# Kernel optimization log

Measured on AMD Instinct MI355X. Metric: run time of the kernel, lower is better.

Reference implementation:

```python
import jax, jax.numpy as jnp
import numpy as np

V, E, C = 50000, 5000, 16
TAU = 0.5
EPS = 1e-08
SPARSITY = 0.02  # fraction of (v,e) incidences


def setup_inputs() -> dict:
    key = jax.random.key(0)
    k1, k2, k3, k4 = jax.random.split(key, 4)
    pred_s = jax.random.normal(k1, (V, C), dtype=jnp.float32)
    pred_t = jax.random.normal(k2, (V, C), dtype=jnp.float32)
    # binary incidence matrix; pin vertex 0 into every edge so deg_e > 0
    H = (jax.random.uniform(k3, (V, E)) < SPARSITY).astype(jnp.float32)
    H = H.at[0, :].set(1.0)
    e_mask = jax.random.randint(k4, (E,), 0, 2).astype(jnp.bool_)
    return {"pred_s": pred_s, "pred_t": pred_t, "H": H, "e_mask": e_mask}


def _v2e_mean(p, H, deg_e):
    # == einsum('vc,ve->ec', p, H @ diag(1/deg_e)) : column-normalized scatter-mean
    return jnp.einsum('ve,vc->ec', H, p) / deg_e[:, None]


def reference(pred_s, pred_t, H, e_mask):
    ps = jax.nn.softmax(pred_s, axis=1)   # [V, C]
    pt = jax.nn.softmax(pred_t, axis=1)   # [V, C]
    deg_e = H.sum(axis=0)                 # [E]
    log_s = jnp.log(_v2e_mean(ps, H, deg_e) / TAU + EPS)  # [E, C]
    log_t = jnp.log(_v2e_mean(pt, H, deg_e) / TAU + EPS)  # [E, C]
    # F.kl_div(input=log_s, target=log_t, log_target=True, reduction='batchmean')
    # restricted to masked edges; mask via weights to keep shapes static.
    kl = jnp.exp(log_t) * (log_t - log_s)                  # [E, C]
    m = e_mask.astype(kl.dtype)                            # [E]
    n_sel = jnp.maximum(m.sum(), 1.0)
    return (kl * m[:, None]).sum() / n_sel
```

## Files before the change

kernel.cpp:

```cpp
#include <hip/hip_runtime.h>

#define NV 50000
#define NE 5000
#define NC 16
#define TAU_INV 2.0f
#define EPS 1e-8f
#define VCHUNK 1000
#define NCHUNK 50

__global__ __launch_bounds__(256) void softmax_kernel(
    const float* __restrict__ pred_s, const float* __restrict__ pred_t,
    float* __restrict__ ps, float* __restrict__ pt) {
  int i = blockIdx.x * 256 + threadIdx.x;
  if (i >= 2 * NV) return;
  const float* src;
  float* dst;
  if (i < NV) { src = pred_s + (size_t)i * NC; dst = ps + (size_t)i * NC; }
  else        { int j = i - NV; src = pred_t + (size_t)j * NC; dst = pt + (size_t)j * NC; }
  float4 a = ((const float4*)src)[0];
  float4 b = ((const float4*)src)[1];
  float4 c = ((const float4*)src)[2];
  float4 d = ((const float4*)src)[3];
  float x[16] = {a.x,a.y,a.z,a.w, b.x,b.y,b.z,b.w, c.x,c.y,c.z,c.w, d.x,d.y,d.z,d.w};
  float mx = x[0];
#pragma unroll
  for (int k = 1; k < 16; ++k) mx = fmaxf(mx, x[k]);
  float sum = 0.f;
#pragma unroll
  for (int k = 0; k < 16; ++k) { x[k] = expf(x[k] - mx); sum += x[k]; }
  float inv = 1.f / sum;
#pragma unroll
  for (int k = 0; k < 16; ++k) x[k] *= inv;
  float4 o0 = {x[0], x[1], x[2], x[3]};
  float4 o1 = {x[4], x[5], x[6], x[7]};
  float4 o2 = {x[8], x[9], x[10], x[11]};
  float4 o3 = {x[12], x[13], x[14], x[15]};
  ((float4*)dst)[0] = o0;
  ((float4*)dst)[1] = o1;
  ((float4*)dst)[2] = o2;
  ((float4*)dst)[3] = o3;
}

__global__ __launch_bounds__(256) void accum_kernel(
    const float* __restrict__ H, const float* __restrict__ ps,
    const float* __restrict__ pt, float* __restrict__ acc) {
  int e = blockIdx.x * 256 + threadIdx.x;
  if (e >= NE) return;
  int v0 = blockIdx.y * VCHUNK;

  float deg = 0.f;
  float as[16], at[16];
#pragma unroll
  for (int k = 0; k < 16; ++k) { as[k] = 0.f; at[k] = 0.f; }

  const float* hp = H + (size_t)v0 * NE + e;
  for (int v = v0; v < v0 + VCHUNK; v += 4) {
    float h0 = hp[0];
    float h1 = hp[NE];
    float h2 = hp[2 * NE];
    float h3 = hp[3 * NE];
    hp += (size_t)4 * NE;
#pragma unroll
    for (int u = 0; u < 4; ++u) {
      float h = (u == 0) ? h0 : (u == 1) ? h1 : (u == 2) ? h2 : h3;
      const float* rs = ps + (size_t)(v + u) * NC;
      const float* rt = pt + (size_t)(v + u) * NC;
      float4 sA = ((const float4*)rs)[0];
      float4 sB = ((const float4*)rs)[1];
      float4 sC = ((const float4*)rs)[2];
      float4 sD = ((const float4*)rs)[3];
      float4 tA = ((const float4*)rt)[0];
      float4 tB = ((const float4*)rt)[1];
      float4 tC = ((const float4*)rt)[2];
      float4 tD = ((const float4*)rt)[3];
      float sv[16] = {sA.x,sA.y,sA.z,sA.w, sB.x,sB.y,sB.z,sB.w,
                      sC.x,sC.y,sC.z,sC.w, sD.x,sD.y,sD.z,sD.w};
      float tv[16] = {tA.x,tA.y,tA.z,tA.w, tB.x,tB.y,tB.z,tB.w,
                      tC.x,tC.y,tC.z,tC.w, tD.x,tD.y,tD.z,tD.w};
      deg += h;
#pragma unroll
      for (int k = 0; k < 16; ++k) as[k] = fmaf(h, sv[k], as[k]);
#pragma unroll
      for (int k = 0; k < 16; ++k) at[k] = fmaf(h, tv[k], at[k]);
    }
  }

  atomicAdd(&acc[e], deg);
#pragma unroll
  for (int k = 0; k < 16; ++k)
    atomicAdd(&acc[NE + (size_t)k * NE + e], as[k]);
#pragma unroll
  for (int k = 0; k < 16; ++k)
    atomicAdd(&acc[(size_t)17 * NE + (size_t)k * NE + e], at[k]);
}

__global__ __launch_bounds__(256) void kl_kernel(
    const float* __restrict__ acc, const unsigned char* __restrict__ e_mask,
    float* __restrict__ out) {
  __shared__ float snum[256];
  __shared__ float scnt[256];
  int t = threadIdx.x;
  float num = 0.f, cnt = 0.f;
  for (int e = t; e < NE; e += 256) {
    if (e_mask[e]) {
      float deg = acc[e];
      float invd = 1.f / deg;
      float kl = 0.f;
#pragma unroll
      for (int k = 0; k < 16; ++k) {
        float ms = acc[NE + (size_t)k * NE + e] * invd;
        float mt = acc[(size_t)17 * NE + (size_t)k * NE + e] * invd;
        float xs = ms * TAU_INV + EPS;
        float xt = mt * TAU_INV + EPS;
        kl += xt * (logf(xt) - logf(xs));
      }
      num += kl;
      cnt += 1.f;
    }
  }
  snum[t] = num;
  scnt[t] = cnt;
  __syncthreads();
  if (t == 0) {
    float n = 0.f, c2 = 0.f;
    for (int k = 0; k < 256; ++k) { n += snum[k]; c2 += scnt[k]; }
    out[0] = n / fmaxf(c2, 1.f);
  }
}

extern "C" void kernel_launch(void* const* d_in, const int* in_sizes, int n_in,
                              void* d_out, int out_size, void* d_ws, size_t ws_size,
                              hipStream_t stream) {
  const float* pred_s = (const float*)d_in[0];
  const float* pred_t = (const float*)d_in[1];
  const float* H      = (const float*)d_in[2];
  const unsigned char* e_mask = (const unsigned char*)d_in[3];

  float* ws = (float*)d_ws;
  float* ps  = ws;
  float* pt  = ws + (size_t)NV * NC;
  float* acc = ws + (size_t)2 * NV * NC;

  hipMemsetAsync(acc, 0, (size_t)33 * NE * sizeof(float), stream);
  softmax_kernel<<<dim3((2 * NV + 255) / 256), 256, 0, stream>>>(pred_s, pred_t, ps, pt);
  accum_kernel<<<dim3((NE + 255) / 256, NCHUNK), 256, 0, stream>>>(H, ps, pt, acc);
  kl_kernel<<<1, 256, 0, stream>>>(acc, e_mask, (float*)d_out);
}
```

Baseline: 1.451 ms.

## Interleave softmax outputs per vertex and simplify accumulation loop

The softmax outputs for the student and teacher predictions are now written into one interleaved buffer of 32 floats per vertex, so the accumulation kernel reads both rows from a single contiguous 128-byte region. The accumulation loop is restructured to step one vertex at a time with unroll 2, and gets a launch-bounds occupancy hint. Out-of-range threads are clamped rather than returning early, so every lane stays active through the loop and only the atomics are guarded. The final KL reduction now uses wavefront shuffles instead of a serial 256-element loop, which is minor next to the dominant read of the dense H matrix.

```diff
diff --git a/kernel.cpp b/kernel.cpp
--- a/kernel.cpp
+++ b/kernel.cpp
@@ -10,13 +10,13 @@
 
 __global__ __launch_bounds__(256) void softmax_kernel(
     const float* __restrict__ pred_s, const float* __restrict__ pred_t,
-    float* __restrict__ ps, float* __restrict__ pt) {
+    float* __restrict__ p) {
   int i = blockIdx.x * 256 + threadIdx.x;
   if (i >= 2 * NV) return;
   const float* src;
   float* dst;
-  if (i < NV) { src = pred_s + (size_t)i * NC; dst = ps + (size_t)i * NC; }
-  else        { int j = i - NV; src = pred_t + (size_t)j * NC; dst = pt + (size_t)j * NC; }
+  if (i < NV) { src = pred_s + (size_t)i * NC; dst = p + (size_t)i * 32; }
+  else        { int j = i - NV; src = pred_t + (size_t)j * NC; dst = p + (size_t)j * 32 + 16; }
   float4 a = ((const float4*)src)[0];
   float4 b = ((const float4*)src)[1];
   float4 c = ((const float4*)src)[2];
@@ -41,11 +41,11 @@
   ((float4*)dst)[3] = o3;
 }
 
-__global__ __launch_bounds__(256) void accum_kernel(
-    const float* __restrict__ H, const float* __restrict__ ps,
-    const float* __restrict__ pt, float* __restrict__ acc) {
-  int e = blockIdx.x * 256 + threadIdx.x;
-  if (e >= NE) return;
+__global__ __launch_bounds__(256, 4) void accum_kernel(
+    const float* __restrict__ H, const float* __restrict__ p,
+    float* __restrict__ acc) {
+  int te = blockIdx.x * 256 + threadIdx.x;
+  int e = te < NE ? te : NE - 1;
   int v0 = blockIdx.y * VCHUNK;
 
   float deg = 0.f;
@@ -53,52 +53,47 @@
 #pragma unroll
   for (int k = 0; k < 16; ++k) { as[k] = 0.f; at[k] = 0.f; }
 
-  const float* hp = H + (size_t)v0 * NE + e;
-  for (int v = v0; v < v0 + VCHUNK; v += 4) {
-    float h0 = hp[0];
-    float h1 = hp[NE];
-    float h2 = hp[2 * NE];
-    float h3 = hp[3 * NE];
-    hp += (size_t)4 * NE;
+  const float* __restrict__ hp = H + (size_t)v0 * NE + e;
+  const float* __restrict__ pp = p + (size_t)v0 * 32;
+
+#pragma unroll 2
+  for (int v = 0; v < VCHUNK; ++v) {
+    float h = hp[(size_t)v * NE];
+    float4 sA = ((const float4*)(pp + (size_t)v * 32))[0];
+    float4 sB = ((const float4*)(pp + (size_t)v * 32))[1];
+    float4 sC = ((const float4*)(pp + (size_t)v * 32))[2];
+    float4 sD = ((const float4*)(pp + (size_t)v * 32))[3];
+    float4 tA = ((const float4*)(pp + (size_t)v * 32))[4];
+    float4 tB = ((const float4*)(pp + (size_t)v * 32))[5];
+    float4 tC = ((const float4*)(pp + (size_t)v * 32))[6];
+    float4 tD = ((const float4*)(pp + (size_t)v * 32))[7];
+    float sv[16] = {sA.x,sA.y,sA.z,sA.w, sB.x,sB.y,sB.z,sB.w,
+                    sC.x,sC.y,sC.z,sC.w, sD.x,sD.y,sD.z,sD.w};
+    float tv[16] = {tA.x,tA.y,tA.z,tA.w, tB.x,tB.y,tB.z,tB.w,
+                    tC.x,tC.y,tC.z,tC.w, tD.x,tD.y,tD.z,tD.w};
+    deg += h;
 #pragma unroll
-    for (int u = 0; u < 4; ++u) {
-      float h = (u == 0) ? h0 : (u == 1) ? h1 : (u == 2) ? h2 : h3;
-      const float* rs = ps + (size_t)(v + u) * NC;
-      const float* rt = pt + (size_t)(v + u) * NC;
-      float4 sA = ((const float4*)rs)[0];
-      float4 sB = ((const float4*)rs)[1];
-      float4 sC = ((const float4*)rs)[2];
-      float4 sD = ((const float4*)rs)[3];
-      float4 tA = ((const float4*)rt)[0];
-      float4 tB = ((const float4*)rt)[1];
-      float4 tC = ((const float4*)rt)[2];
-      float4 tD = ((const float4*)rt)[3];
-      float sv[16] = {sA.x,sA.y,sA.z,sA.w, sB.x,sB.y,sB.z,sB.w,
-                      sC.x,sC.y,sC.z,sC.w, sD.x,sD.y,sD.z,sD.w};
-      float tv[16] = {tA.x,tA.y,tA.z,tA.w, tB.x,tB.y,tB.z,tB.w,
-                      tC.x,tC.y,tC.z,tC.w, tD.x,tD.y,tD.z,tD.w};
-      deg += h;
+    for (int k = 0; k < 16; ++k) as[k] = fmaf(h, sv[k], as[k]);
 #pragma unroll
-      for (int k = 0; k < 16; ++k) as[k] = fmaf(h, sv[k], as[k]);
-#pragma unroll
-      for (int k = 0; k < 16; ++k) at[k] = fmaf(h, tv[k], at[k]);
-    }
+    for (int k = 0; k < 16; ++k) at[k] = fmaf(h, tv[k], at[k]);
   }
 
-  atomicAdd(&acc[e], deg);
+  if (te < NE) {
+    atomicAdd(&acc[e], deg);
 #pragma unroll
-  for (int k = 0; k < 16; ++k)
-    atomicAdd(&acc[NE + (size_t)k * NE + e], as[k]);
+    for (int k = 0; k < 16; ++k)
+      atomicAdd(&acc[NE + (size_t)k * NE + e], as[k]);
 #pragma unroll
-  for (int k = 0; k < 16; ++k)
-    atomicAdd(&acc[(size_t)17 * NE + (size_t)k * NE + e], at[k]);
+    for (int k = 0; k < 16; ++k)
+      atomicAdd(&acc[(size_t)17 * NE + (size_t)k * NE + e], at[k]);
+  }
 }
 
 __global__ __launch_bounds__(256) void kl_kernel(
     const float* __restrict__ acc, const unsigned char* __restrict__ e_mask,
     float* __restrict__ out) {
-  __shared__ float snum[256];
-  __shared__ float scnt[256];
+  __shared__ float snum[4];
+  __shared__ float scnt[4];
   int t = threadIdx.x;
   float num = 0.f, cnt = 0.f;
   for (int e = t; e < NE; e += 256) {
@@ -118,12 +113,16 @@
       cnt += 1.f;
     }
   }
-  snum[t] = num;
-  scnt[t] = cnt;
+#pragma unroll
+  for (int off = 32; off > 0; off >>= 1) {
+    num += __shfl_down(num, off, 64);
+    cnt += __shfl_down(cnt, off, 64);
+  }
+  if ((t & 63) == 0) { snum[t >> 6] = num; scnt[t >> 6] = cnt; }
   __syncthreads();
   if (t == 0) {
-    float n = 0.f, c2 = 0.f;
-    for (int k = 0; k < 256; ++k) { n += snum[k]; c2 += scnt[k]; }
+    float n = snum[0] + snum[1] + snum[2] + snum[3];
+    float c2 = scnt[0] + scnt[1] + scnt[2] + scnt[3];
     out[0] = n / fmaxf(c2, 1.f);
   }
 }
@@ -137,12 +136,11 @@
   const unsigned char* e_mask = (const unsigned char*)d_in[3];
 
   float* ws = (float*)d_ws;
-  float* ps  = ws;
-  float* pt  = ws + (size_t)NV * NC;
-  float* acc = ws + (size_t)2 * NV * NC;
+  float* p   = ws;
+  float* acc = ws + (size_t)NV * 32;
 
   hipMemsetAsync(acc, 0, (size_t)33 * NE * sizeof(float), stream);
-  softmax_kernel<<<dim3((2 * NV + 255) / 256), 256, 0, stream>>>(pred_s, pred_t, ps, pt);
-  accum_kernel<<<dim3((NE + 255) / 256, NCHUNK), 256, 0, stream>>>(H, ps, pt, acc);
+  softmax_kernel<<<dim3((2 * NV + 255) / 256), 256, 0, stream>>>(pred_s, pred_t, p);
+  accum_kernel<<<dim3((NE + 255) / 256, NCHUNK), 256, 0, stream>>>(H, p, acc);
   kl_kernel<<<1, 256, 0, stream>>>(acc, e_mask, (float*)d_out);
 }
```

Result: no change. 1.448 ms (-0.2%).
